# Kernel optimization log

Measured on AMD Instinct MI355X. Metric: run time of the kernel, lower is better.

The kernel has to match this reference:

```python
import jax, jax.numpy as jnp
import numpy as np

# Scaled Llama backbone (NF4 dequant-matmul == dense matmul math) + LoRA(q,v) + cls head
L, V, D, H, F, R, C = 4, 32000, 2048, 16, 8192, 16, 3
HD = D // H  # 128, matches real Llama head_dim
ALPHA_OVER_R = 32.0 / R
EPS = 1e-5
NEG = -1e9


def setup_inputs() -> dict:
    B, S = 2, 1024
    keys = iter(jax.random.split(jax.random.key(0), 40))

    def rn(shape, s=0.02):
        return jax.random.normal(next(keys), shape, dtype=jnp.float32) * s

    return {
        "input_ids": jax.random.randint(next(keys), (B, S), 0, V),
        "attention_mask": jnp.ones((B, S), dtype=jnp.int32),
        "embed": rn((V, D)),
        "Wq": rn((L, D, D)), "Wk": rn((L, D, D)), "Wv": rn((L, D, D)), "Wo": rn((L, D, D)),
        "Aq": rn((L, R, D)), "Bq": rn((L, D, R)), "Av": rn((L, R, D)), "Bv": rn((L, D, R)),
        "Wg": rn((L, F, D)), "Wu": rn((L, F, D)), "Wd": rn((L, D, F)),
        "norm1": jnp.ones((L, D)), "norm2": jnp.ones((L, D)), "final_norm": jnp.ones((D,)),
        "head_W1": rn((D, D)), "head_b1": jnp.zeros((D,)),
        "head_W2": rn((C, D)), "head_b2": jnp.zeros((C,)),
    }


def _rms(x, w):
    return x * w * jax.lax.rsqrt(jnp.mean(x * x, -1, keepdims=True) + EPS)


def _rope_tables(S):
    inv = 1.0 / (10000.0 ** (jnp.arange(0, HD, 2, dtype=jnp.float32) / HD))
    f = jnp.outer(jnp.arange(S, dtype=jnp.float32), inv)  # [S, HD//2]
    emb = jnp.concatenate([f, f], -1)                      # [S, HD]
    return jnp.cos(emb), jnp.sin(emb)


def _rot(x):
    return jnp.concatenate([-x[..., HD // 2:], x[..., :HD // 2]], -1)


def reference(input_ids, attention_mask, embed, Wq, Wk, Wv, Wo, Aq, Bq, Av, Bv,
              Wg, Wu, Wd, norm1, norm2, final_norm, head_W1, head_b1, head_W2, head_b2):
    B, S = input_ids.shape
    x = embed[input_ids]                                   # [B,S,D]
    cos, sin = _rope_tables(S)
    causal = jnp.tril(jnp.ones((S, S), dtype=bool))
    mask = jnp.where(causal[None, None], 0.0, NEG) \
        + (1.0 - attention_mask.astype(jnp.float32))[:, None, None, :] * NEG  # [B,1,S,S]

    for l in range(L):  # small fixed layer count
        h = _rms(x, norm1[l])

        def proj(W):
            return jnp.einsum('bsd,ed->bse', h, W)

        def lora(A, Bm):
            return ALPHA_OVER_R * jnp.einsum('bsr,er->bse', jnp.einsum('bsd,rd->bsr', h, A), Bm)

        q = (proj(Wq[l]) + lora(Aq[l], Bq[l])).reshape(B, S, H, HD)
        k = proj(Wk[l]).reshape(B, S, H, HD)
        v = (proj(Wv[l]) + lora(Av[l], Bv[l])).reshape(B, S, H, HD)
        q = q * cos[None, :, None, :] + _rot(q) * sin[None, :, None, :]
        k = k * cos[None, :, None, :] + _rot(k) * sin[None, :, None, :]

        scores = jnp.einsum('bqhd,bkhd->bhqk', q, k) / np.float32(np.sqrt(HD)) + mask
        attn = jax.nn.softmax(scores, -1)
        o = jnp.einsum('bhqk,bkhd->bqhd', attn, v).reshape(B, S, D)
        x = x + jnp.einsum('bsd,ed->bse', o, Wo[l])

        h2 = _rms(x, norm2[l])
        g = jnp.einsum('bsd,fd->bsf', h2, Wg[l])
        u = jnp.einsum('bsd,fd->bsf', h2, Wu[l])
        x = x + jnp.einsum('bsf,df->bsd', jax.nn.silu(g) * u, Wd[l])

    x = _rms(x, final_norm)
    # LlamaForSequenceClassification pooling at last non-pad token; score = Identity
    idx = jnp.sum(attention_mask, -1) - 1
    pooled = x[jnp.arange(B), idx].astype(jnp.float32)     # [B, D]
    # head_layer (dropout = identity in eval)
    h = jnp.tanh(pooled @ head_W1.T + head_b1)
    return h @ head_W2.T + head_b2                          # [B, C]
```

## Files before the change

### kernel.cpp

```cpp
#include <hip/hip_runtime.h>

#define NLAYER 4
#define DMODEL 2048
#define NHEAD  16
#define HEADD  128
#define FFDIM  8192
#define RLORA  16
#define SEQLEN 1024
#define NBATCH 2
#define NTOK   (NBATCH*SEQLEN)
#define QKVS   6144

typedef __bf16 bf16x8 __attribute__((ext_vector_type(8)));
typedef float  f32x4  __attribute__((ext_vector_type(4)));
typedef unsigned short us8 __attribute__((ext_vector_type(8)));

__device__ __forceinline__ unsigned short f2b(float f) {
  unsigned int u = __builtin_bit_cast(unsigned int, f);
  u += 0x7FFFu + ((u >> 16) & 1u);
  return (unsigned short)(u >> 16);
}
__device__ __forceinline__ float b2f(unsigned short s) {
  unsigned int u = ((unsigned int)s) << 16;
  return __builtin_bit_cast(float, u);
}
__device__ __forceinline__ int vswz(int d) {
  return (((d >> 2) & 7) ^ ((d & 3) << 1)) << 4;
}
typedef __attribute__((address_space(1))) const void* gas_t;
typedef __attribute__((address_space(3))) void* las_t;
__device__ __forceinline__ void gload16(const void* g, void* l) {
  __builtin_amdgcn_global_load_lds((gas_t)g, (las_t)l, 16, 0, 0);
}

__global__ void k_embed(const int* __restrict__ ids, const float* __restrict__ emb,
                        float* __restrict__ x) {
  int row = blockIdx.x;
  int id = ids[row];
  const float4* src = (const float4*)(emb + (size_t)id * DMODEL);
  float4* dst = (float4*)(x + (size_t)row * DMODEL);
  for (int i = threadIdx.x; i < DMODEL / 4; i += 256) dst[i] = src[i];
}

__global__ void k_cvt16(const float* __restrict__ s, unsigned short* __restrict__ d, int n8) {
  int stride = gridDim.x * 256;
  for (int i = blockIdx.x * 256 + threadIdx.x; i < n8; i += stride) {
    size_t si = (size_t)i * 2;
    float4 a = ((const float4*)s)[si];
    float4 b = ((const float4*)s)[si + 1];
    us8 o;
    o[0]=f2b(a.x); o[1]=f2b(a.y); o[2]=f2b(a.z); o[3]=f2b(a.w);
    o[4]=f2b(b.x); o[5]=f2b(b.y); o[6]=f2b(b.z); o[7]=f2b(b.w);
    ((us8*)d)[i] = o;
  }
}

__global__ void k_cvtqkv(const float* __restrict__ Wq, const float* __restrict__ Wk,
                         const float* __restrict__ Wv, unsigned short* __restrict__ d) {
  const size_t DD8 = (size_t)DMODEL * DMODEL / 8;
  const int n8 = (int)(NLAYER * 3 * DD8);
  int stride = gridDim.x * 256;
  for (int i = blockIdx.x * 256 + threadIdx.x; i < n8; i += stride) {
    int blk = i >> 19;
    int lay = blk / 3;
    int ten = blk - lay * 3;
    int off = i & ((1 << 19) - 1);
    const float* s = (ten == 0 ? Wq : ten == 1 ? Wk : Wv) + (size_t)lay * DMODEL * DMODEL;
    float4 a = ((const float4*)s)[(size_t)off * 2];
    float4 b = ((const float4*)s)[(size_t)off * 2 + 1];
    us8 o;
    o[0]=f2b(a.x); o[1]=f2b(a.y); o[2]=f2b(a.z); o[3]=f2b(a.w);
    o[4]=f2b(b.x); o[5]=f2b(b.y); o[6]=f2b(b.z); o[7]=f2b(b.w);
    ((us8*)(d))[(size_t)i] = o;
  }
}

__global__ void k_rmsnorm(const float* __restrict__ x, const float* __restrict__ w,
                          unsigned short* __restrict__ h) {
  int row = blockIdx.x, t = threadIdx.x;
  const float* xr = x + (size_t)row * DMODEL;
  float4 a = ((const float4*)xr)[t];
  float4 b = ((const float4*)xr)[t + 256];
  float ss = a.x*a.x + a.y*a.y + a.z*a.z + a.w*a.w
           + b.x*b.x + b.y*b.y + b.z*b.z + b.w*b.w;
  for (int m = 32; m; m >>= 1) ss += __shfl_xor(ss, m);
  __shared__ float red[4];
  if ((t & 63) == 0) red[t >> 6] = ss;
  __syncthreads();
  ss = red[0] + red[1] + red[2] + red[3];
  float rs = rsqrtf(ss * (1.0f / DMODEL) + 1e-5f);
  float4 wa = ((const float4*)w)[t];
  float4 wb = ((const float4*)w)[t + 256];
  ushort4 oa, ob;
  oa.x = f2b(a.x * wa.x * rs); oa.y = f2b(a.y * wa.y * rs);
  oa.z = f2b(a.z * wa.z * rs); oa.w = f2b(a.w * wa.w * rs);
  ob.x = f2b(b.x * wb.x * rs); ob.y = f2b(b.y * wb.y * rs);
  ob.z = f2b(b.z * wb.z * rs); ob.w = f2b(b.w * wb.w * rs);
  ushort4* hr = (ushort4*)(h + (size_t)row * DMODEL);
  hr[t] = oa;
  hr[t + 256] = ob;
}

__global__ __launch_bounds__(512, 4)
void k_ffn(const unsigned short* __restrict__ A, const unsigned short* __restrict__ Bgw,
           const unsigned short* __restrict__ Buw, unsigned short* __restrict__ act,
           int N, int K, int ldc) {
  __shared__ unsigned short As[8192];
  __shared__ unsigned short Gs[8192];
  __shared__ unsigned short Us[8192];
  const int t = threadIdx.x, l = t & 63, w = t >> 6;
  const int wm = w >> 2, wn = w & 3;
  const int nbx = gridDim.x;
  const int nmt = gridDim.y;
  const int nwg = nbx * nmt;
  const int bid = blockIdx.y * nbx + blockIdx.x;
  const int sid = (bid & 7) * (nwg >> 3) + (bid >> 3);
  const int m0 = (sid % nmt) << 7;
  const int n0 = (sid / nmt) << 7;
  const int srow = (w << 3) + (l >> 3);
  const int gcol = 8 * ((l & 7) ^ ((srow >> 1) & 7));
  const unsigned short* Ap = A   + (size_t)(m0 + srow) * K + gcol;
  const unsigned short* Gp = Bgw + (size_t)(n0 + srow) * K + gcol;
  const unsigned short* Up = Buw + (size_t)(n0 + srow) * K + gcol;
  const size_t r64K = (size_t)64 * K;
  unsigned short* AsW = As + (w << 9);
  unsigned short* GsW = Gs + (w << 9);
  unsigned short* UsW = Us + (w << 9);
  const int cl = l & 15, lh = l >> 4;
  const int fR = (cl >> 1) & 7;
  f32x4 ag[4][2], au[4][2];
  #pragma unroll
  for (int mi = 0; mi < 4; mi++)
    #pragma unroll
    for (int ni = 0; ni < 2; ni++) {
      f32x4 z = {0.f,0.f,0.f,0.f};
      ag[mi][ni] = z; au[mi][ni] = z;
    }

  for (int kt = 0; kt < K; kt += 64) {
    gload16(Ap + kt,          AsW);
    gload16(Ap + kt + r64K,   AsW + 4096);
    gload16(Gp + kt,          GsW);
    gload16(Gp + kt + r64K,   GsW + 4096);
    gload16(Up + kt,          UsW);
    gload16(Up + kt + r64K,   UsW + 4096);
    __syncthreads();
    #pragma unroll
    for (int kh = 0; kh < 2; kh++) {
      const int so = ((kh * 4 + lh) ^ fR) << 4;
      bf16x8 af[4], bg[2], bu[2];
      #pragma unroll
      for (int mi = 0; mi < 4; mi++)
        af[mi] = *(const bf16x8*)((const char*)As + (wm*64 + mi*16 + cl) * 128 + so);
      #pragma unroll
      for (int ni = 0; ni < 2; ni++) {
        bg[ni] = *(const bf16x8*)((const char*)Gs + (wn*32 + ni*16 + cl) * 128 + so);
        bu[ni] = *(const bf16x8*)((const char*)Us + (wn*32 + ni*16 + cl) * 128 + so);
      }
      #pragma unroll
      for (int mi = 0; mi < 4; mi++)
        #pragma unroll
        for (int ni = 0; ni < 2; ni++) {
          ag[mi][ni] = __builtin_amdgcn_mfma_f32_16x16x32_bf16(af[mi], bg[ni], ag[mi][ni], 0, 0, 0);
          au[mi][ni] = __builtin_amdgcn_mfma_f32_16x16x32_bf16(af[mi], bu[ni], au[mi][ni], 0, 0, 0);
        }
    }
    __syncthreads();
  }
  const int rbase = lh << 2;
  #pragma unroll
  for (int mi = 0; mi < 4; mi++) {
    #pragma unroll
    for (int ni = 0; ni < 2; ni++) {
      #pragma unroll
      for (int rr = 0; rr < 4; rr++) {
        int row = m0 + wm * 64 + mi * 16 + rbase + rr;
        int col = n0 + wn * 32 + ni * 16 + cl;
        float gv = ag[mi][ni][rr];
        float uv = au[mi][ni][rr];
        float val = gv / (1.0f + __expf(-gv)) * uv;
        act[(size_t)row * ldc + col] = f2b(val);
      }
    }
  }
}

template<int MODE>
__global__ __launch_bounds__(256, 4)
void k_gemm6(const unsigned short* __restrict__ A, const unsigned short* __restrict__ B,
             float* __restrict__ Cf, unsigned short* __restrict__ Cb,
             const float* __restrict__ Res, const unsigned short* __restrict__ Gaux,
             int N, int K, int ldc) {
  __shared__ unsigned short As[8192];
  __shared__ unsigned short Bs[16384];
  const int t = threadIdx.x, l = t & 63, w = t >> 6;
  const int nbx = gridDim.x;
  const int nmt = gridDim.y;
  const int bid = blockIdx.y * nbx + blockIdx.x;
  const int xcd = bid & 7;
  const int local = bid >> 3;
  const int cm = nmt >> 2;
  const int cn = nbx >> 1;
  const int m0 = ((xcd & 3) * cm + (local % cm)) << 6;
  const int n0 = ((xcd >> 2) * cn + (local / cm)) << 7;
  const int srow = (w << 2) + (l >> 4);
  const int gcol = 8 * ((l & 15) ^ ((srow >> 1) & 7));
  const unsigned short* Ag = A + (size_t)(m0 + srow) * K + gcol;
  const unsigned short* Bg = B + (size_t)(n0 + srow) * K + gcol;
  const size_t r16K = (size_t)16 * K;
  unsigned short* AsW = As + (w << 9);
  unsigned short* BsW = Bs + (w << 9);
  const int cl = l & 15, lh = l >> 4;
  const int fR = (cl >> 1) & 7;
  f32x4 acc[4][2];
  #pragma unroll
  for (int mi = 0; mi < 4; mi++)
    #pragma unroll
    for (int ni = 0; ni < 2; ni++) { f32x4 z = {0.f,0.f,0.f,0.f}; acc[mi][ni] = z; }

  for (int kt = 0; kt < K; kt += 128) {
    gload16(Ag + kt,          AsW);
    gload16(Ag + kt +   r16K, AsW + 2048);
    gload16(Ag + kt + 2*r16K, AsW + 4096);
    gload16(Ag + kt + 3*r16K, AsW + 6144);
    gload16(Bg + kt,          BsW);
    gload16(Bg + kt +   r16K, BsW + 2048);
    gload16(Bg + kt + 2*r16K, BsW + 4096);
    gload16(Bg + kt + 3*r16K, BsW + 6144);
    gload16(Bg + kt + 4*r16K, BsW + 8192);
    gload16(Bg + kt + 5*r16K, BsW + 10240);
    gload16(Bg + kt + 6*r16K, BsW + 12288);
    gload16(Bg + kt + 7*r16K, BsW + 14336);
    __syncthreads();
    #pragma unroll
    for (int kk = 0; kk < 4; kk++) {
      const int so = ((kk * 4 + lh) ^ fR) << 4;
      bf16x8 af[4], bf[2];
      #pragma unroll
      for (int mi = 0; mi < 4; mi++)
        af[mi] = *(const bf16x8*)((const char*)As + (mi*16 + cl) * 256 + so);
      #pragma unroll
      for (int ni = 0; ni < 2; ni++)
        bf[ni] = *(const bf16x8*)((const char*)Bs + (w*32 + ni*16 + cl) * 256 + so);
      #pragma unroll
      for (int mi = 0; mi < 4; mi++)
        #pragma unroll
        for (int ni = 0; ni < 2; ni++)
          acc[mi][ni] = __builtin_amdgcn_mfma_f32_16x16x32_bf16(af[mi], bf[ni], acc[mi][ni], 0, 0, 0);
    }
    __syncthreads();
  }
  const int rbase = lh << 2;
  #pragma unroll
  for (int mi = 0; mi < 4; mi++) {
    #pragma unroll
    for (int ni = 0; ni < 2; ni++) {
      #pragma unroll
      for (int rr = 0; rr < 4; rr++) {
        int row = m0 + mi * 16 + rbase + rr;
        int col = n0 + w * 32 + ni * 16 + cl;
        size_t idx = (size_t)row * ldc + col;
        float val = acc[mi][ni][rr];
        if constexpr (MODE == 0) Cf[idx] = val;
        if constexpr (MODE == 1) Cf[idx] = val + Res[idx];
        if constexpr (MODE == 2) Cb[idx] = f2b(val);
        if constexpr (MODE == 3) {
          float gv = b2f(Gaux[idx]);
          val *= gv / (1.0f + __expf(-gv));
          Cb[idx] = f2b(val);
        }
      }
    }
  }
}

__global__ __launch_bounds__(256, 4)
void k_gemm7(const unsigned short* __restrict__ A, const unsigned short* __restrict__ B,
             unsigned short* __restrict__ qb, unsigned short* __restrict__ kb,
             unsigned short* __restrict__ vb,
             const float* __restrict__ ct, const float* __restrict__ st,
             int K,
             const float* __restrict__ ltq, const float* __restrict__ ltv,
             const float* __restrict__ lbq, const float* __restrict__ lbv) {
  __shared__ unsigned short As[4096];
  __shared__ unsigned short Bs[8192];
  const int t = threadIdx.x, l = t & 63, w = t >> 6;
  const int nbx = gridDim.x;
  const int nmt = gridDim.y;
  const int nwg = nbx * nmt;
  const int bid = blockIdx.y * nbx + blockIdx.x;
  const int sid = (bid & 7) * (nwg >> 3) + (bid >> 3);
  const int m0 = (sid % nmt) << 6;
  const int n0 = (sid / nmt) << 7;
  const int srow = (w << 3) + (l >> 3);
  const int gcol = 8 * ((l & 7) ^ ((srow >> 1) & 7));
  const unsigned short* Ag = A + (size_t)(m0 + srow) * K + gcol;
  const unsigned short* Bg = B + (size_t)(n0 + srow) * K + gcol;
  const size_t r32K = (size_t)32 * K;
  unsigned short* AsW = As + (w << 9);
  unsigned short* BsW = Bs + (w << 9);
  const int cl = l & 15, lh = l >> 4;
  const int fR = (cl >> 1) & 7;
  f32x4 acc[4][2];
  #pragma unroll
  for (int mi = 0; mi < 4; mi++)
    #pragma unroll
    for (int ni = 0; ni < 2; ni++) { f32x4 z = {0.f,0.f,0.f,0.f}; acc[mi][ni] = z; }

  for (int kt = 0; kt < K; kt += 64) {
    gload16(Ag + kt,          AsW);
    gload16(Ag + kt +   r32K, AsW + 2048);
    gload16(Bg + kt,          BsW);
    gload16(Bg + kt +   r32K, BsW + 2048);
    gload16(Bg + kt + 2*r32K, BsW + 4096);
    gload16(Bg + kt + 3*r32K, BsW + 6144);
    __syncthreads();
    #pragma unroll
    for (int kh = 0; kh < 2; kh++) {
      const int so = ((kh * 4 + lh) ^ fR) << 4;
      bf16x8 af[4], bf[2];
      #pragma unroll
      for (int mi = 0; mi < 4; mi++)
        af[mi] = *(const bf16x8*)((const char*)As + (mi*16 + cl) * 128 + so);
      #pragma unroll
      for (int ni = 0; ni < 2; ni++)
        bf[ni] = *(const bf16x8*)((const char*)Bs + (w*16 + ni*64 + cl) * 128 + so);
      #pragma unroll
      for (int mi = 0; mi < 4; mi++)
        #pragma unroll
        for (int ni = 0; ni < 2; ni++)
          acc[mi][ni] = __builtin_amdgcn_mfma_f32_16x16x32_bf16(af[mi], bf[ni], acc[mi][ni], 0, 0, 0);
    }
    __syncthreads();
  }
  const int rbase = lh << 2;
  const int i0 = (w << 4) + cl;
  const int col_lo = n0 + i0;
  const int reg = n0 >> 11;
  const float* lt = nullptr;
  const float* lb_lo = nullptr;
  const float* lb_hi = nullptr;
  if (reg == 0)      { lt = ltq; lb_lo = lbq + (size_t)col_lo * RLORA;
                                 lb_hi = lbq + (size_t)(col_lo + 64) * RLORA; }
  else if (reg == 2) { lt = ltv; lb_lo = lbv + (size_t)(col_lo - 4096) * RLORA;
                                 lb_hi = lbv + (size_t)(col_lo - 4096 + 64) * RLORA; }
  float4 bl0={0,0,0,0}, bl1=bl0, bl2=bl0, bl3=bl0;
  float4 bh0=bl0, bh1=bl0, bh2=bl0, bh3=bl0;
  if (lt) {
    bl0 = ((const float4*)lb_lo)[0]; bl1 = ((const float4*)lb_lo)[1];
    bl2 = ((const float4*)lb_lo)[2]; bl3 = ((const float4*)lb_lo)[3];
    bh0 = ((const float4*)lb_hi)[0]; bh1 = ((const float4*)lb_hi)[1];
    bh2 = ((const float4*)lb_hi)[2]; bh3 = ((const float4*)lb_hi)[3];
  }
  unsigned short* outp = (reg == 0 ? qb : reg == 1 ? kb : vb);
  const int ocol = col_lo - reg * 2048;
  #pragma unroll
  for (int mi = 0; mi < 4; mi++) {
    #pragma unroll
    for (int rr = 0; rr < 4; rr++) {
      int row = m0 + mi * 16 + rbase + rr;
      float lo = acc[mi][0][rr];
      float hi = acc[mi][1][rr];
      if (lt) {
        const float4* tr = (const float4*)(lt + (size_t)row * RLORA);
        float4 t0 = tr[0], t1 = tr[1], t2 = tr[2], t3 = tr[3];
        lo += 2.0f * (t0.x*bl0.x + t0.y*bl0.y + t0.z*bl0.z + t0.w*bl0.w
                    + t1.x*bl1.x + t1.y*bl1.y + t1.z*bl1.z + t1.w*bl1.w
                    + t2.x*bl2.x + t2.y*bl2.y + t2.z*bl2.z + t2.w*bl2.w
                    + t3.x*bl3.x + t3.y*bl3.y + t3.z*bl3.z + t3.w*bl3.w);
        hi += 2.0f * (t0.x*bh0.x + t0.y*bh0.y + t0.z*bh0.z + t0.w*bh0.w
                    + t1.x*bh1.x + t1.y*bh1.y + t1.z*bh1.z + t1.w*bh1.w
                    + t2.x*bh2.x + t2.y*bh2.y + t2.z*bh2.z + t2.w*bh2.w
                    + t3.x*bh3.x + t3.y*bh3.y + t3.z*bh3.z + t3.w*bh3.w);
      }
      if (reg != 2) {
        int s = row & (SEQLEN - 1);
        float c = ct[s * 64 + i0], sn = st[s * 64 + i0];
        float nlo = lo * c - hi * sn;
        float nhi = hi * c + lo * sn;
        lo = nlo; hi = nhi;
      }
      outp[(size_t)row * DMODEL + ocol]      = f2b(lo);
      outp[(size_t)row * DMODEL + ocol + 64] = f2b(hi);
    }
  }
}

template<int MODE>
__global__ __launch_bounds__(256, 2)
void k_gemm(const unsigned short* __restrict__ A, const void* __restrict__ Bv,
            float* __restrict__ Cf, unsigned short* __restrict__ Cb,
            const float* __restrict__ Res, const unsigned short* __restrict__ Gaux,
            int N, int K, int ldc) {
  __shared__ unsigned char lds[128 * 32 * 2 * 2];
  unsigned char* As = lds;
  unsigned char* Bs = lds + 128 * 32 * 2;
  const int t = threadIdx.x;
  const int l = t & 63, w = t >> 6;
  const int wr = w >> 1, wc = w & 1;
  const int m0 = blockIdx.y << 7, n0 = blockIdx.x << 7;
  const int sr = t >> 1, skh = (t & 1) << 4;
  const int sByte = sr * 64 + (skh << 1);
  const int sSwz = (sr & 3) << 4;
  const unsigned short* Ap = A + (size_t)(m0 + sr) * K + skh;
  const float* Bp32 = (const float*)Bv + (size_t)(n0 + sr) * K + skh;
  const int kOff = (((l >> 4) << 4)) ^ ((l & 3) << 4);
  const int arow = wr * 64 + (l & 15);
  const int brow = wc * 64 + (l & 15);
  f32x4 acc[4][4];
  #pragma unroll
  for (int mi = 0; mi < 4; mi++)
    #pragma unroll
    for (int ni = 0; ni < 4; ni++) { f32x4 z = {0.f,0.f,0.f,0.f}; acc[mi][ni] = z; }

  for (int kt = 0; kt < K; kt += 32) {
    uint4 a0 = *(const uint4*)(Ap + kt);
    uint4 a1 = *(const uint4*)(Ap + kt + 8);
    *(uint4*)(As + ((sByte)      ^ sSwz)) = a0;
    *(uint4*)(As + ((sByte + 16) ^ sSwz)) = a1;
    float4 f0 = *(const float4*)(Bp32 + kt);
    float4 f1 = *(const float4*)(Bp32 + kt + 4);
    float4 f2 = *(const float4*)(Bp32 + kt + 8);
    float4 f3 = *(const float4*)(Bp32 + kt + 12);
    us8 q0, q1;
    q0[0]=f2b(f0.x); q0[1]=f2b(f0.y); q0[2]=f2b(f0.z); q0[3]=f2b(f0.w);
    q0[4]=f2b(f1.x); q0[5]=f2b(f1.y); q0[6]=f2b(f1.z); q0[7]=f2b(f1.w);
    q1[0]=f2b(f2.x); q1[1]=f2b(f2.y); q1[2]=f2b(f2.z); q1[3]=f2b(f2.w);
    q1[4]=f2b(f3.x); q1[5]=f2b(f3.y); q1[6]=f2b(f3.z); q1[7]=f2b(f3.w);
    *(us8*)(Bs + ((sByte)      ^ sSwz)) = q0;
    *(us8*)(Bs + ((sByte + 16) ^ sSwz)) = q1;
    __syncthreads();
    bf16x8 af[4], bfr[4];
    #pragma unroll
    for (int i = 0; i < 4; i++) {
      af[i]  = *(const bf16x8*)(As + (arow + 16 * i) * 64 + kOff);
      bfr[i] = *(const bf16x8*)(Bs + (brow + 16 * i) * 64 + kOff);
    }
    #pragma unroll
    for (int mi = 0; mi < 4; mi++)
      #pragma unroll
      for (int ni = 0; ni < 4; ni++)
        acc[mi][ni] = __builtin_amdgcn_mfma_f32_16x16x32_bf16(af[mi], bfr[ni], acc[mi][ni], 0, 0, 0);
    __syncthreads();
  }
  const int rbase = (l >> 4) << 2;
  const int cl = l & 15;
  #pragma unroll
  for (int mi = 0; mi < 4; mi++) {
    #pragma unroll
    for (int ni = 0; ni < 4; ni++) {
      #pragma unroll
      for (int rr = 0; rr < 4; rr++) {
        int row = m0 + wr * 64 + mi * 16 + rbase + rr;
        int col = n0 + wc * 64 + ni * 16 + cl;
        size_t idx = (size_t)row * ldc + col;
        float val = acc[mi][ni][rr];
        if constexpr (MODE == 0) Cf[idx] = val;
        if constexpr (MODE == 1) Cf[idx] = val + Res[idx];
        if constexpr (MODE == 2) Cb[idx] = f2b(val);
        if constexpr (MODE == 3) {
          float gv = b2f(Gaux[idx]);
          val *= gv / (1.0f + __expf(-gv));
          Cb[idx] = f2b(val);
        }
      }
    }
  }
}

__global__ void k_lora_down2(const unsigned short* __restrict__ h,
                             const float* __restrict__ Aq, const float* __restrict__ Av,
                             float* __restrict__ tbq, float* __restrict__ tbv) {
  int t = threadIdx.x;
  int m = blockIdx.x * 8 + (t >> 5), r = t & 31;
  const float* ar = (r < 16) ? (Aq + (size_t)r * DMODEL)
                             : (Av + (size_t)(r - 16) * DMODEL);
  const unsigned short* hr = h + (size_t)m * DMODEL;
  float acc = 0.f;
  for (int d = 0; d < DMODEL; d += 4) {
    ushort4 hv = *(const ushort4*)(hr + d);
    float4 av = *(const float4*)(ar + d);
    acc += b2f(hv.x)*av.x + b2f(hv.y)*av.y + b2f(hv.z)*av.z + b2f(hv.w)*av.w;
  }
  if (r < 16) tbq[(size_t)m * RLORA + r] = acc;
  else        tbv[(size_t)m * RLORA + (r - 16)] = acc;
}

__global__ void k_lora_down(const unsigned short* __restrict__ h, const float* __restrict__ Am,
                            float* __restrict__ tb) {
  int t = threadIdx.x;
  int m = blockIdx.x * 16 + (t >> 4), r = t & 15;
  const unsigned short* hr = h + (size_t)m * DMODEL;
  const float* ar = Am + (size_t)r * DMODEL;
  float acc = 0.f;
  for (int d = 0; d < DMODEL; d += 4) {
    ushort4 hv = *(const ushort4*)(hr + d);
    float4 av = *(const float4*)(ar + d);
    acc += b2f(hv.x)*av.x + b2f(hv.y)*av.y + b2f(hv.z)*av.z + b2f(hv.w)*av.w;
  }
  tb[(size_t)m * RLORA + r] = acc;
}

__global__ void k_lora_up(const float* __restrict__ tb, const float* __restrict__ Bm,
                          float* __restrict__ out, int ldc) {
  int tid = blockIdx.x * 256 + threadIdx.x;
  int m = tid >> 11, e = tid & (DMODEL - 1);
  const float* tr = tb + (size_t)m * RLORA;
  const float* br = Bm + (size_t)e * RLORA;
  float acc = 0.f;
  #pragma unroll
  for (int r = 0; r < RLORA; r += 4) {
    float4 tv = *(const float4*)(tr + r);
    float4 bv = *(const float4*)(br + r);
    acc += tv.x*bv.x + tv.y*bv.y + tv.z*bv.z + tv.w*bv.w;
  }
  out[(size_t)m * ldc + e] += 2.0f * acc;
}

__global__ void k_rope_table(float* __restrict__ ct, float* __restrict__ st) {
  int tid = blockIdx.x * 256 + threadIdx.x;
  int s = tid >> 6, i = tid & 63;
  float inv = __expf(-((float)i / 64.0f) * logf(10000.0f));
  float ang = (float)s * inv;
  ct[tid] = cosf(ang);
  st[tid] = sinf(ang);
}

__global__ void k_rope2(const float* __restrict__ qkv,
                        const float* __restrict__ ct, const float* __restrict__ st,
                        unsigned short* __restrict__ qb, unsigned short* __restrict__ kb,
                        unsigned short* __restrict__ vb) {
  int tid = blockIdx.x * 256 + threadIdx.x;
  int i = tid & 63;
  int hh = (tid >> 6) & (NHEAD - 1);
  int s = (tid >> 10) & (SEQLEN - 1);
  int b = tid >> 20;
  size_t ibase = ((size_t)(b * SEQLEN + s)) * QKVS + hh * HEADD;
  size_t obase = ((size_t)(b * SEQLEN + s)) * DMODEL + hh * HEADD;
  float c = ct[s * 64 + i], sn = st[s * 64 + i];
  float q0 = qkv[ibase + i], q1 = qkv[ibase + i + 64];
  qb[obase + i]      = f2b(q0 * c - q1 * sn);
  qb[obase + i + 64] = f2b(q1 * c + q0 * sn);
  float k0 = qkv[ibase + 2048 + i], k1 = qkv[ibase + 2048 + i + 64];
  kb[obase + i]      = f2b(k0 * c - k1 * sn);
  kb[obase + i + 64] = f2b(k1 * c + k0 * sn);
  vb[obase + i]      = f2b(qkv[ibase + 4096 + i]);
  vb[obase + i + 64] = f2b(qkv[ibase + 4096 + i + 64]);
}

__global__ __launch_bounds__(256, 2)
void k_attn_bf16(const unsigned short* __restrict__ qbp, const unsigned short* __restrict__ kbp,
                 const unsigned short* __restrict__ vbp, const int* __restrict__ am,
                 unsigned short* __restrict__ o, int vstride) {
  __shared__ unsigned char Kls[64 * 256];
  __shared__ unsigned char Vls[128 * 128];
  __shared__ unsigned char Pls[64 * 128];
  const int qt = blockIdx.x, hh = blockIdx.y, b = blockIdx.z;
  const int t = threadIdx.x, l = t & 63, w = t >> 6;
  const int cl = l & 15, lh = l >> 4;
  const int rbase = lh << 2;
  const int prow = t >> 4;
  const int pc   = t & 15;

  #pragma unroll
  for (int ii = 0; ii < 4; ii++) {
    int row = prow + 16 * ii;
    uint4 u = *(const uint4*)(qbp + ((size_t)(b*SEQLEN + qt*64 + row)) * DMODEL + hh * HEADD + pc * 8);
    *(uint4*)(Kls + ((row * 256 + pc * 16) ^ ((row & 7) << 4))) = u;
  }
  uint4 kreg[4], vreg[4];
  #pragma unroll
  for (int ii = 0; ii < 4; ii++) {
    int row = prow + 16 * ii;
    kreg[ii] = *(const uint4*)(kbp + ((size_t)(b*SEQLEN + row)) * DMODEL + hh * HEADD + pc * 8);
    vreg[ii] = *(const uint4*)(vbp + ((size_t)(b*SEQLEN + row)) * vstride + hh * HEADD + pc * 8);
  }
  __syncthreads();
  bf16x8 qf[4];
  {
    int row = w * 16 + cl;
    int swz = (row & 7) << 4;
    #pragma unroll
    for (int kt = 0; kt < 4; kt++)
      qf[kt] = *(const bf16x8*)(Kls + ((row * 256 + kt * 64 + lh * 16) ^ swz));
  }

  f32x4 oacc[8];
  #pragma unroll
  for (int i = 0; i < 8; i++) { f32x4 z = {0.f,0.f,0.f,0.f}; oacc[i] = z; }
  float mrun[4], lrun[4];
  #pragma unroll
  for (int r = 0; r < 4; r++) { mrun[r] = -3e38f; lrun[r] = 0.f; }

  for (int kb = 0; kb <= qt; kb++) {
    __syncthreads();
    #pragma unroll
    for (int ii = 0; ii < 4; ii++) {
      int row = prow + 16 * ii;
      *(uint4*)(Kls + ((row * 256 + pc * 16) ^ ((row & 7) << 4))) = kreg[ii];
    }
    #pragma unroll
    for (int ii = 0; ii < 4; ii++) {
      int n = prow + 16 * ii;
      uint4 a = vreg[ii];
      uint4 p;
      p.x = __shfl_xor(a.x, 16); p.y = __shfl_xor(a.y, 16);
      p.z = __shfl_xor(a.z, 16); p.w = __shfl_xor(a.w, 16);
      if (!(l & 16)) {
        int d0 = pc * 8, nb = n * 2;
        unsigned int wd[8];
        wd[0] = (a.x & 0xffffu) | (p.x << 16);
        wd[1] = (a.x >> 16)     | (p.x & 0xffff0000u);
        wd[2] = (a.y & 0xffffu) | (p.y << 16);
        wd[3] = (a.y >> 16)     | (p.y & 0xffff0000u);
        wd[4] = (a.z & 0xffffu) | (p.z << 16);
        wd[5] = (a.z >> 16)     | (p.z & 0xffff0000u);
        wd[6] = (a.w & 0xffffu) | (p.w << 16);
        wd[7] = (a.w >> 16)     | (p.w & 0xffff0000u);
        #pragma unroll
        for (int e = 0; e < 8; e++)
          *(unsigned int*)(Vls + (((d0 + e) * 128 + nb) ^ vswz(d0 + e))) = wd[e];
      }
    }
    __syncthreads();
    if (kb < qt) {
      #pragma unroll
      for (int ii = 0; ii < 4; ii++) {
        int row = prow + 16 * ii;
        kreg[ii] = *(const uint4*)(kbp + ((size_t)(b*SEQLEN + (kb+1)*64 + row)) * DMODEL + hh * HEADD + pc * 8);
        vreg[ii] = *(const uint4*)(vbp + ((size_t)(b*SEQLEN + (kb+1)*64 + row)) * vstride + hh * HEADD + pc * 8);
      }
    }
    f32x4 sacc[4];
    #pragma unroll
    for (int nt = 0; nt < 4; nt++) { f32x4 z = {0.f,0.f,0.f,0.f}; sacc[nt] = z; }
    #pragma unroll
    for (int kt = 0; kt < 4; kt++) {
      #pragma unroll
      for (int nt = 0; nt < 4; nt++) {
        int row = nt * 16 + cl;
        bf16x8 kf = *(const bf16x8*)(Kls + ((row * 256 + kt * 64 + lh * 16) ^ ((row & 7) << 4)));
        sacc[nt] = __builtin_amdgcn_mfma_f32_16x16x32_bf16(qf[kt], kf, sacc[nt], 0, 0, 0);
      }
    }
    float p[4][4];
    float mt[4] = {-3e38f, -3e38f, -3e38f, -3e38f};
    #pragma unroll
    for (int nt = 0; nt < 4; nt++) {
      int kg = kb * 64 + nt * 16 + cl;
      float pad = (1.0f - (float)am[b * SEQLEN + kg]) * (-1e9f);
      #pragma unroll
      for (int r = 0; r < 4; r++) {
        int qg = qt * 64 + w * 16 + rbase + r;
        float s = sacc[nt][r] * 0.08838834764831845f + pad;
        if (kg > qg) s = -1e30f;
        p[nt][r] = s;
        mt[r] = fmaxf(mt[r], s);
      }
    }
    #pragma unroll
    for (int r = 0; r < 4; r++) {
      float m = mt[r];
      m = fmaxf(m, __shfl_xor(m, 1)); m = fmaxf(m, __shfl_xor(m, 2));
      m = fmaxf(m, __shfl_xor(m, 4)); m = fmaxf(m, __shfl_xor(m, 8));
      mt[r] = m;
    }
    float corr[4];
    #pragma unroll
    for (int r = 0; r < 4; r++) {
      float mnew = fmaxf(mrun[r], mt[r]);
      corr[r] = __expf(mrun[r] - mnew);
      mrun[r] = mnew;
    }
    float ps[4] = {0.f, 0.f, 0.f, 0.f};
    #pragma unroll
    for (int nt = 0; nt < 4; nt++)
      #pragma unroll
      for (int r = 0; r < 4; r++) {
        p[nt][r] = __expf(p[nt][r] - mrun[r]);
        ps[r] += p[nt][r];
      }
    #pragma unroll
    for (int r = 0; r < 4; r++) {
      float s = ps[r];
      s += __shfl_xor(s, 1); s += __shfl_xor(s, 2);
      s += __shfl_xor(s, 4); s += __shfl_xor(s, 8);
      lrun[r] = lrun[r] * corr[r] + s;
    }
    #pragma unroll
    for (int nt = 0; nt < 4; nt++)
      #pragma unroll
      for (int r = 0; r < 4; r++) {
        int row = w * 16 + rbase + r;
        *(unsigned short*)(Pls + ((row * 128 + (nt * 16 + cl) * 2) ^ ((row & 7) << 4))) = f2b(p[nt][r]);
      }
    #pragma unroll
    for (int dt = 0; dt < 8; dt++)
      #pragma unroll
      for (int r = 0; r < 4; r++) oacc[dt][r] *= corr[r];
    {
      int prw = w * 16 + cl, pswz = (prw & 7) << 4;
      bf16x8 pf0 = *(const bf16x8*)(Pls + ((prw * 128 +  0 + lh * 16) ^ pswz));
      bf16x8 pf1 = *(const bf16x8*)(Pls + ((prw * 128 + 64 + lh * 16) ^ pswz));
      #pragma unroll
      for (int dt = 0; dt < 8; dt++) {
        int drow = dt * 16 + cl;
        bf16x8 vf0 = *(const bf16x8*)(Vls + ((drow * 128 +  0 + lh * 16) ^ vswz(drow)));
        bf16x8 vf1 = *(const bf16x8*)(Vls + ((drow * 128 + 64 + lh * 16) ^ vswz(drow)));
        oacc[dt] = __builtin_amdgcn_mfma_f32_16x16x32_bf16(pf0, vf0, oacc[dt], 0, 0, 0);
        oacc[dt] = __builtin_amdgcn_mfma_f32_16x16x32_bf16(pf1, vf1, oacc[dt], 0, 0, 0);
      }
    }
  }
  size_t obase = (((size_t)b * SEQLEN + qt * 64 + w * 16) * NHEAD + hh) * HEADD;
  #pragma unroll
  for (int r = 0; r < 4; r++) {
    float inv = 1.0f / lrun[r];
    int row = rbase + r;
    #pragma unroll
    for (int dt = 0; dt < 8; dt++)
      o[obase + (size_t)row * (NHEAD * HEADD) + dt * 16 + cl] = f2b(oacc[dt][r] * inv);
  }
}

__global__ void k_pool(const float* __restrict__ x, const int* __restrict__ am,
                       const float* __restrict__ fn, float* __restrict__ pooled) {
  int b = blockIdx.x, t = threadIdx.x;
  __shared__ float red[4];
  float fc = 0.f;
  for (int i = t; i < SEQLEN; i += 256) fc += (float)am[b * SEQLEN + i];
  for (int m = 32; m; m >>= 1) fc += __shfl_xor(fc, m);
  if ((t & 63) == 0) red[t >> 6] = fc;
  __syncthreads();
  int idx = (int)(red[0] + red[1] + red[2] + red[3]) - 1;
  const float* xr = x + ((size_t)b * SEQLEN + idx) * DMODEL;
  float4 a = ((const float4*)xr)[t], c = ((const float4*)xr)[t + 256];
  float ss = a.x*a.x + a.y*a.y + a.z*a.z + a.w*a.w
           + c.x*c.x + c.y*c.y + c.z*c.z + c.w*c.w;
  for (int m = 32; m; m >>= 1) ss += __shfl_xor(ss, m);
  __syncthreads();
  if ((t & 63) == 0) red[t >> 6] = ss;
  __syncthreads();
  ss = red[0] + red[1] + red[2] + red[3];
  float rs = rsqrtf(ss * (1.0f / DMODEL) + 1e-5f);
  float4 w0 = ((const float4*)fn)[t], w1 = ((const float4*)fn)[t + 256];
  float4 o0, o1;
  o0.x = a.x*rs*w0.x; o0.y = a.y*rs*w0.y; o0.z = a.z*rs*w0.z; o0.w = a.w*rs*w0.w;
  o1.x = c.x*rs*w1.x; o1.y = c.y*rs*w1.y; o1.z = c.z*rs*w1.z; o1.w = c.w*rs*w1.w;
  ((float4*)(pooled + (size_t)b * DMODEL))[t] = o0;
  ((float4*)(pooled + (size_t)b * DMODEL))[t + 256] = o1;
}

__global__ void k_head1(const float* __restrict__ pooled, const float* __restrict__ W1,
                        const float* __restrict__ b1, float* __restrict__ h1) {
  int bi = blockIdx.x;
  int b = bi >> 3, e = ((bi & 7) << 8) + threadIdx.x;
  const float* pr = pooled + (size_t)b * DMODEL;
  const float* wr = W1 + (size_t)e * DMODEL;
  float acc = 0.f;
  for (int d = 0; d < DMODEL; d += 4) {
    float4 pv = *(const float4*)(pr + d);
    float4 wv = *(const float4*)(wr + d);
    acc += pv.x*wv.x + pv.y*wv.y + pv.z*wv.z + pv.w*wv.w;
  }
  h1[(size_t)b * DMODEL + e] = tanhf(acc + b1[e]);
}

__global__ void k_head2(const float* __restrict__ h1, const float* __restrict__ W2,
                        const float* __restrict__ b2, float* __restrict__ out) {
  int bi = blockIdx.x;
  int b = bi / 3, c = bi % 3;
  int l = threadIdx.x;
  float acc = 0.f;
  for (int e = l; e < DMODEL; e += 64)
    acc += h1[(size_t)b * DMODEL + e] * W2[(size_t)c * DMODEL + e];
  for (int m = 32; m; m >>= 1) acc += __shfl_xor(acc, m);
  if (l == 0) out[b * 3 + c] = acc + b2[c];
}

__global__ void k_sentinel(float* out) {
  if (threadIdx.x < 6) out[threadIdx.x] = -12345.0f;
}

extern "C" void kernel_launch(void* const* d_in, const int* in_sizes, int n_in,
                              void* d_out, int out_size, void* d_ws, size_t ws_size,
                              hipStream_t stream) {
  const int*   ids = (const int*)d_in[0];
  const int*   am  = (const int*)d_in[1];
  const float* emb = (const float*)d_in[2];
  const float* Wq  = (const float*)d_in[3];
  const float* Wk  = (const float*)d_in[4];
  const float* Wv  = (const float*)d_in[5];
  const float* Wo  = (const float*)d_in[6];
  const float* Aq  = (const float*)d_in[7];
  const float* Bq  = (const float*)d_in[8];
  const float* Av  = (const float*)d_in[9];
  const float* Bv  = (const float*)d_in[10];
  const float* Wg  = (const float*)d_in[11];
  const float* Wu  = (const float*)d_in[12];
  const float* Wd  = (const float*)d_in[13];
  const float* n1  = (const float*)d_in[14];
  const float* n2  = (const float*)d_in[15];
  const float* fn  = (const float*)d_in[16];
  const float* hW1 = (const float*)d_in[17];
  const float* hb1 = (const float*)d_in[18];
  const float* hW2 = (const float*)d_in[19];
  const float* hb2 = (const float*)d_in[20];
  float* out = (float*)d_out;

  const size_t XOFF    = 0;
  const size_t HOFF    = 16777216;
  const size_t QBOFF   = 25165824;
  const size_t KBOFF   = 33554432;
  const size_t VBOFF   = 41943040;
  const size_t OOFF    = 50331648;
  const size_t GOFF    = 58720256;
  const size_t ACTOFF  = 92274688;
  const size_t QKV32OFF= 125829120;
  const size_t TOFF    = 176160768;
  const size_t NEED = TOFF + 131072 + 131072 + 262144 + 262144 + 16384 + 16384;
  if (ws_size < NEED) {
    k_sentinel<<<1, 64, 0, stream>>>(out);
    return;
  }
  const size_t W16OFF   = (NEED + 255) & ~(size_t)255;
  const size_t W16BYTES = 536870912ull;
  const bool   use16    = ws_size >= W16OFF + W16BYTES;

  char* ws = (char*)d_ws;
  float*          x     = (float*)(ws + XOFF);
  unsigned short* h     = (unsigned short*)(ws + HOFF);
  unsigned short* qb    = (unsigned short*)(ws + QBOFF);
  unsigned short* kb    = (unsigned short*)(ws + KBOFF);
  unsigned short* vb    = (unsigned short*)(ws + VBOFF);
  unsigned short* o     = (unsigned short*)(ws + OOFF);
  unsigned short* g     = (unsigned short*)(ws + GOFF);
  unsigned short* act   = (unsigned short*)(ws + ACTOFF);
  float*          qkv32 = (float*)(ws + QKV32OFF);
  float* tbq    = (float*)(ws + TOFF);
  float* tbv    = (float*)(ws + TOFF + 131072);
  float* ct     = (float*)(ws + TOFF + 262144);
  float* st     = (float*)(ws + TOFF + 262144 + 262144);
  float* pooled = (float*)(ws + TOFF + 262144 + 524288);
  float* h1     = (float*)(ws + TOFF + 262144 + 524288 + 16384);

  unsigned short* w16 = (unsigned short*)(ws + W16OFF);
  const size_t DD = (size_t)DMODEL * DMODEL;
  const size_t FD = (size_t)FFDIM * DMODEL;
  unsigned short* wqkv16 = w16;
  unsigned short* wo16   = w16 + 4ull * 3 * DD;
  unsigned short* wg16   = wo16 + 4ull * DD;
  unsigned short* wu16   = wg16 + 4ull * FD;
  unsigned short* wd16   = wu16 + 4ull * FD;
  if (use16) {
    k_cvtqkv<<<2048, 256, 0, stream>>>(Wq, Wk, Wv, wqkv16);
    k_cvt16<<<2048, 256, 0, stream>>>(Wo, wo16, (int)(4 * DD / 8));
    k_cvt16<<<2048, 256, 0, stream>>>(Wg, wg16, (int)(4 * FD / 8));
    k_cvt16<<<2048, 256, 0, stream>>>(Wu, wu16, (int)(4 * FD / 8));
    k_cvt16<<<2048, 256, 0, stream>>>(Wd, wd16, (int)(4 * FD / 8));
  }

  k_embed<<<NTOK, 256, 0, stream>>>(ids, emb, x);
  k_rope_table<<<SEQLEN * 64 / 256, 256, 0, stream>>>(ct, st);

  dim3 g16(16, 16), gqkv(48, 32), gffn(64, 16), gsq(16, 32), ga(SEQLEN / 64, NHEAD, NBATCH);
  for (int lay = 0; lay < NLAYER; lay++) {
    const float* Bq_l = Bq + (size_t)lay * DMODEL * RLORA;
    const float* Bv_l = Bv + (size_t)lay * DMODEL * RLORA;
    k_rmsnorm<<<NTOK, 256, 0, stream>>>(x, n1 + (size_t)lay * DMODEL, h);
    if (use16) {
      k_lora_down2<<<NTOK / 8, 256, 0, stream>>>(h, Aq + (size_t)lay * RLORA * DMODEL,
                                                 Av + (size_t)lay * RLORA * DMODEL, tbq, tbv);
      k_gemm7<<<gqkv, 256, 0, stream>>>(h, wqkv16 + lay*3*DD, qb, kb, vb, ct, st,
                                        DMODEL, tbq, tbv, Bq_l, Bv_l);
      k_attn_bf16<<<ga, 256, 0, stream>>>(qb, kb, vb, am, o, DMODEL);
      k_gemm6<1><<<gsq, 256, 0, stream>>>(o, wo16 + lay*DD, x, nullptr, x, nullptr, DMODEL, DMODEL, DMODEL);
      k_rmsnorm<<<NTOK, 256, 0, stream>>>(x, n2 + (size_t)lay * DMODEL, h);
      k_ffn<<<gffn, 512, 0, stream>>>(h, wg16 + lay*FD, wu16 + lay*FD, act, FFDIM, DMODEL, FFDIM);
      k_gemm6<1><<<gsq, 256, 0, stream>>>(act, wd16 + lay*FD, x, nullptr, x, nullptr, DMODEL, FFDIM, DMODEL);
    } else {
      k_lora_down<<<NTOK / 16, 256, 0, stream>>>(h, Aq + (size_t)lay * RLORA * DMODEL, tbq);
      k_lora_down<<<NTOK / 16, 256, 0, stream>>>(h, Av + (size_t)lay * RLORA * DMODEL, tbv);
      k_gemm<0><<<g16, 256, 0, stream>>>(h, Wq + lay*DD, qkv32,        nullptr, nullptr, nullptr, DMODEL, DMODEL, QKVS);
      k_gemm<0><<<g16, 256, 0, stream>>>(h, Wk + lay*DD, qkv32 + 2048, nullptr, nullptr, nullptr, DMODEL, DMODEL, QKVS);
      k_gemm<0><<<g16, 256, 0, stream>>>(h, Wv + lay*DD, qkv32 + 4096, nullptr, nullptr, nullptr, DMODEL, DMODEL, QKVS);
      k_lora_up<<<NTOK * DMODEL / 256, 256, 0, stream>>>(tbq, Bq_l, qkv32, QKVS);
      k_lora_up<<<NTOK * DMODEL / 256, 256, 0, stream>>>(tbv, Bv_l, qkv32 + 4096, QKVS);
      k_rope2<<<NBATCH * SEQLEN * NHEAD * 64 / 256, 256, 0, stream>>>(qkv32, ct, st, qb, kb, vb);
      k_attn_bf16<<<ga, 256, 0, stream>>>(qb, kb, vb, am, o, DMODEL);
      k_gemm<1><<<g16, 256, 0, stream>>>(o, Wo + lay*DD, x, nullptr, x, nullptr, DMODEL, DMODEL, DMODEL);
      k_rmsnorm<<<NTOK, 256, 0, stream>>>(x, n2 + (size_t)lay * DMODEL, h);
      k_gemm<2><<<dim3(64,16), 256, 0, stream>>>(h, Wg + lay*FD, nullptr, g, nullptr, nullptr, FFDIM, DMODEL, FFDIM);
      k_gemm<3><<<dim3(64,16), 256, 0, stream>>>(h, Wu + lay*FD, nullptr, act, nullptr, g, FFDIM, DMODEL, FFDIM);
      k_gemm<1><<<g16, 256, 0, stream>>>(act, Wd + lay*FD, x, nullptr, x, nullptr, DMODEL, FFDIM, DMODEL);
    }
  }
  k_pool<<<NBATCH, 256, 0, stream>>>(x, am, fn, pooled);
  k_head1<<<16, 256, 0, stream>>>(pooled, hW1, hb1, h1);
  k_head2<<<6, 64, 0, stream>>>(h1, hW2, hb2, out);
}
```

Measured before the change: 2.507 ms.

## Split fused gate/up FFN into two double-buffered 256x256 GEMMs

Replaces the fused gate+up FFN kernel, which used 128x128 tiles with single-buffered LDS, by a new 256x256-tile GEMM template. It has double-buffered LDS, prefetches the next K tile interleaved with MFMA quarters, and raises MFMA priority with setprio. The gate GEMM now writes g to memory, and the up GEMM reads it back to apply SiLU in its epilogue. The larger tiles and the overlap target better operand reuse and hiding of load latency. The cost is an extra round trip of the g intermediate through memory, reading h twice, and fewer workgroups (256) with higher register and LDS pressure.

```diff
diff --git a/kernel.cpp b/kernel.cpp
--- a/kernel.cpp
+++ b/kernel.cpp
@@ -101,13 +101,13 @@
   hr[t + 256] = ob;
 }
 
-__global__ __launch_bounds__(512, 4)
-void k_ffn(const unsigned short* __restrict__ A, const unsigned short* __restrict__ Bgw,
-           const unsigned short* __restrict__ Buw, unsigned short* __restrict__ act,
-           int N, int K, int ldc) {
-  __shared__ unsigned short As[8192];
-  __shared__ unsigned short Gs[8192];
-  __shared__ unsigned short Us[8192];
+template<int MODE>
+__global__ __launch_bounds__(512, 2)
+void k_gemm8(const unsigned short* __restrict__ A, const unsigned short* __restrict__ B,
+             unsigned short* __restrict__ Cb, const unsigned short* __restrict__ Gaux,
+             int N, int K, int ldc) {
+  __shared__ unsigned short LA[2][16384];
+  __shared__ unsigned short LB[2][16384];
   const int t = threadIdx.x, l = t & 63, w = t >> 6;
   const int wm = w >> 2, wn = w & 3;
   const int nbx = gridDim.x;
@@ -115,71 +115,105 @@
   const int nwg = nbx * nmt;
   const int bid = blockIdx.y * nbx + blockIdx.x;
   const int sid = (bid & 7) * (nwg >> 3) + (bid >> 3);
-  const int m0 = (sid % nmt) << 7;
-  const int n0 = (sid / nmt) << 7;
-  const int srow = (w << 3) + (l >> 3);
-  const int gcol = 8 * ((l & 7) ^ ((srow >> 1) & 7));
-  const unsigned short* Ap = A   + (size_t)(m0 + srow) * K + gcol;
-  const unsigned short* Gp = Bgw + (size_t)(n0 + srow) * K + gcol;
-  const unsigned short* Up = Buw + (size_t)(n0 + srow) * K + gcol;
+  const int m0 = (sid % nmt) << 8;
+  const int n0 = (sid / nmt) << 8;
+  const int srow = t >> 3;
+  const int gcol = 8 * ((t & 7) ^ ((srow >> 1) & 7));
+  const unsigned short* Ag = A + (size_t)(m0 + srow) * K + gcol;
+  const unsigned short* Bg = B + (size_t)(n0 + srow) * K + gcol;
   const size_t r64K = (size_t)64 * K;
-  unsigned short* AsW = As + (w << 9);
-  unsigned short* GsW = Gs + (w << 9);
-  unsigned short* UsW = Us + (w << 9);
+  const size_t r128K = (size_t)128 * K;
   const int cl = l & 15, lh = l >> 4;
   const int fR = (cl >> 1) & 7;
-  f32x4 ag[4][2], au[4][2];
-  #pragma unroll
-  for (int mi = 0; mi < 4; mi++)
-    #pragma unroll
-    for (int ni = 0; ni < 2; ni++) {
-      f32x4 z = {0.f,0.f,0.f,0.f};
-      ag[mi][ni] = z; au[mi][ni] = z;
-    }
-
-  for (int kt = 0; kt < K; kt += 64) {
-    gload16(Ap + kt,          AsW);
-    gload16(Ap + kt + r64K,   AsW + 4096);
-    gload16(Gp + kt,          GsW);
-    gload16(Gp + kt + r64K,   GsW + 4096);
-    gload16(Up + kt,          UsW);
-    gload16(Up + kt + r64K,   UsW + 4096);
-    __syncthreads();
-    #pragma unroll
-    for (int kh = 0; kh < 2; kh++) {
-      const int so = ((kh * 4 + lh) ^ fR) << 4;
-      bf16x8 af[4], bg[2], bu[2];
+  f32x4 acc[8][4];
+  #pragma unroll
+  for (int mi = 0; mi < 8; mi++)
+    #pragma unroll
+    for (int ni = 0; ni < 4; ni++) { f32x4 z = {0.f,0.f,0.f,0.f}; acc[mi][ni] = z; }
+
+#define STG_A(d, kt, hh_) do {                                               \
+    const unsigned short* p_ = Ag + (size_t)(kt) * 64 + (size_t)(hh_) * r128K; \
+    unsigned short* l_ = &LA[d][(hh_) * 8192 + (w << 9)];                    \
+    gload16(p_,        l_);                                                  \
+    gload16(p_ + r64K, l_ + 4096);                                           \
+  } while (0)
+#define STG_B(d, kt, hh_) do {                                               \
+    const unsigned short* p_ = Bg + (size_t)(kt) * 64 + (size_t)(hh_) * r128K; \
+    unsigned short* l_ = &LB[d][(hh_) * 8192 + (w << 9)];                    \
+    gload16(p_,        l_);                                                  \
+    gload16(p_ + r64K, l_ + 4096);                                           \
+  } while (0)
+
+  const int NT = K >> 6;
+  STG_A(0, 0, 0); STG_A(0, 0, 1); STG_B(0, 0, 0); STG_B(0, 0, 1);
+  asm volatile("s_waitcnt vmcnt(0)" ::: "memory");
+  __builtin_amdgcn_sched_barrier(0);
+  __builtin_amdgcn_s_barrier();
+  __builtin_amdgcn_sched_barrier(0);
+
+  for (int t0 = 0; t0 < NT; ++t0) {
+    const int cur = t0 & 1, nxt = cur ^ 1;
+    const char* Ab = (const char*)&LA[cur][0];
+    const char* Bb = (const char*)&LB[cur][0];
+    const bool more = (t0 + 1 < NT);
+    #pragma unroll
+    for (int q = 0; q < 4; ++q) {
+      const int mh = q & 1, kk = q >> 1;
+      const int so = ((kk * 4 + lh) ^ fR) << 4;
+      bf16x8 af[4], bf[4];
       #pragma unroll
       for (int mi = 0; mi < 4; mi++)
-        af[mi] = *(const bf16x8*)((const char*)As + (wm*64 + mi*16 + cl) * 128 + so);
-      #pragma unroll
-      for (int ni = 0; ni < 2; ni++) {
-        bg[ni] = *(const bf16x8*)((const char*)Gs + (wn*32 + ni*16 + cl) * 128 + so);
-        bu[ni] = *(const bf16x8*)((const char*)Us + (wn*32 + ni*16 + cl) * 128 + so);
-      }
+        af[mi] = *(const bf16x8*)(Ab + (wm*128 + mh*64 + mi*16 + cl) * 128 + so);
+      #pragma unroll
+      for (int ni = 0; ni < 4; ni++)
+        bf[ni] = *(const bf16x8*)(Bb + (wn*64 + ni*16 + cl) * 128 + so);
+      if (more) {
+        if      (q == 0) STG_A(nxt, t0 + 1, 0);
+        else if (q == 1) STG_A(nxt, t0 + 1, 1);
+        else if (q == 2) STG_B(nxt, t0 + 1, 0);
+        else             STG_B(nxt, t0 + 1, 1);
+      }
+      __builtin_amdgcn_sched_barrier(0);
+      __builtin_amdgcn_s_barrier();
+      asm volatile("s_waitcnt lgkmcnt(0)" ::: "memory");
+      __builtin_amdgcn_sched_barrier(0);
+      __builtin_amdgcn_s_setprio(1);
       #pragma unroll
       for (int mi = 0; mi < 4; mi++)
         #pragma unroll
-        for (int ni = 0; ni < 2; ni++) {
-          ag[mi][ni] = __builtin_amdgcn_mfma_f32_16x16x32_bf16(af[mi], bg[ni], ag[mi][ni], 0, 0, 0);
-          au[mi][ni] = __builtin_amdgcn_mfma_f32_16x16x32_bf16(af[mi], bu[ni], au[mi][ni], 0, 0, 0);
+        for (int ni = 0; ni < 4; ni++)
+          acc[mh*4 + mi][ni] =
+            __builtin_amdgcn_mfma_f32_16x16x32_bf16(af[mi], bf[ni], acc[mh*4 + mi][ni], 0, 0, 0);
+      __builtin_amdgcn_s_setprio(0);
+      __builtin_amdgcn_sched_barrier(0);
+      __builtin_amdgcn_s_barrier();
+      __builtin_amdgcn_sched_barrier(0);
+    }
+    if (more) {
+      asm volatile("s_waitcnt vmcnt(0)" ::: "memory");
+      __builtin_amdgcn_sched_barrier(0);
+      __builtin_amdgcn_s_barrier();
+      __builtin_amdgcn_sched_barrier(0);
+    }
+  }
+#undef STG_A
+#undef STG_B
+  const int rbase = lh << 2;
+  #pragma unroll
+  for (int mi = 0; mi < 8; mi++) {
+    #pragma unroll
+    for (int ni = 0; ni < 4; ni++) {
+      #pragma unroll
+      for (int rr = 0; rr < 4; rr++) {
+        int row = m0 + wm * 128 + mi * 16 + rbase + rr;
+        int col = n0 + wn * 64 + ni * 16 + cl;
+        size_t idx = (size_t)row * ldc + col;
+        float val = acc[mi][ni][rr];
+        if constexpr (MODE == 3) {
+          float gv = b2f(Gaux[idx]);
+          val *= gv / (1.0f + __expf(-gv));
         }
-    }
-    __syncthreads();
-  }
-  const int rbase = lh << 2;
-  #pragma unroll
-  for (int mi = 0; mi < 4; mi++) {
-    #pragma unroll
-    for (int ni = 0; ni < 2; ni++) {
-      #pragma unroll
-      for (int rr = 0; rr < 4; rr++) {
-        int row = m0 + wm * 64 + mi * 16 + rbase + rr;
-        int col = n0 + wn * 32 + ni * 16 + cl;
-        float gv = ag[mi][ni][rr];
-        float uv = au[mi][ni][rr];
-        float val = gv / (1.0f + __expf(-gv)) * uv;
-        act[(size_t)row * ldc + col] = f2b(val);
+        Cb[idx] = f2b(val);
       }
     }
   }
@@ -863,7 +897,7 @@
   k_embed<<<NTOK, 256, 0, stream>>>(ids, emb, x);
   k_rope_table<<<SEQLEN * 64 / 256, 256, 0, stream>>>(ct, st);
 
-  dim3 g16(16, 16), gqkv(48, 32), gffn(64, 16), gsq(16, 32), ga(SEQLEN / 64, NHEAD, NBATCH);
+  dim3 g16(16, 16), gqkv(48, 32), gff8(32, 8), gsq(16, 32), ga(SEQLEN / 64, NHEAD, NBATCH);
   for (int lay = 0; lay < NLAYER; lay++) {
     const float* Bq_l = Bq + (size_t)lay * DMODEL * RLORA;
     const float* Bv_l = Bv + (size_t)lay * DMODEL * RLORA;
@@ -876,7 +910,8 @@
       k_attn_bf16<<<ga, 256, 0, stream>>>(qb, kb, vb, am, o, DMODEL);
       k_gemm6<1><<<gsq, 256, 0, stream>>>(o, wo16 + lay*DD, x, nullptr, x, nullptr, DMODEL, DMODEL, DMODEL);
       k_rmsnorm<<<NTOK, 256, 0, stream>>>(x, n2 + (size_t)lay * DMODEL, h);
-      k_ffn<<<gffn, 512, 0, stream>>>(h, wg16 + lay*FD, wu16 + lay*FD, act, FFDIM, DMODEL, FFDIM);
+      k_gemm8<2><<<gff8, 512, 0, stream>>>(h, wg16 + lay*FD, g,   nullptr, FFDIM, DMODEL, FFDIM);
+      k_gemm8<3><<<gff8, 512, 0, stream>>>(h, wu16 + lay*FD, act, g,       FFDIM, DMODEL, FFDIM);
       k_gemm6<1><<<gsq, 256, 0, stream>>>(act, wd16 + lay*FD, x, nullptr, x, nullptr, DMODEL, FFDIM, DMODEL);
     } else {
       k_lora_down<<<NTOK / 16, 256, 0, stream>>>(h, Aq + (size_t)lay * RLORA * DMODEL, tbq);
```

Result: slower. 2.667 ms (+6.4%).
